# Kernel optimization log

Measured on AMD Instinct MI355X. Metric: run time of the kernel, lower is better.

The kernel has to match this reference:

```python
import jax, jax.numpy as jnp
import numpy as np

N = 50000   # nodes
E = 400000  # edges
IN_DIM, H1, H2, OUT_DIM = 512, 256, 62, 128


def _param(key, shape, scale=0.05):
    return jax.random.normal(key, shape, dtype=jnp.float32) * scale


def setup_inputs() -> dict:
    key = jax.random.key(0)
    ks = jax.random.split(key, 24)
    x = jax.random.normal(ks[0], (N, IN_DIM), dtype=jnp.float32)
    edge_index_neg = jax.random.randint(ks[1], (2, E), 0, N, dtype=jnp.int64)
    d = {
        "x": x, "edge_index_neg": edge_index_neg,
        # nn.Linear params (W stored as [in, out])
        "W1": _param(ks[2], (IN_DIM, H1)), "b1": _param(ks[3], (H1,)),
        "W2": _param(ks[4], (H1, H2)),    "b2": _param(ks[5], (H2,)),
        "W3": _param(ks[6], (H2, OUT_DIM)), "b3": _param(ks[7], (OUT_DIM,)),
        # GCNConv params: lin weight (no bias) + post-aggregation bias
        "Wg1": _param(ks[8], (H1, H1)),   "bg1": _param(ks[9], (H1,)),
        "Wg2": _param(ks[10], (H2, H2)),  "bg2": _param(ks[11], (H2,)),
        "Wg3": _param(ks[12], (OUT_DIM, OUT_DIM)), "bg3": _param(ks[13], (OUT_DIM,)),
        "Wg4": _param(ks[14], (OUT_DIM, OUT_DIM)), "bg4": _param(ks[15], (OUT_DIM,)),
        "Wg5": _param(ks[16], (OUT_DIM, OUT_DIM)), "bg5": _param(ks[17], (OUT_DIM,)),
        "Wg6": _param(ks[18], (OUT_DIM, OUT_DIM)), "bg6": _param(ks[19], (OUT_DIM,)),
    }
    return d


def _build_norm(edge_index):
    # PyG GCNConv: add self-loops, symmetric normalization D^-1/2 A D^-1/2
    loop = jnp.arange(N, dtype=edge_index.dtype)
    src = jnp.concatenate([edge_index[0], loop])
    dst = jnp.concatenate([edge_index[1], loop])
    deg = jax.ops.segment_sum(jnp.ones_like(dst, dtype=jnp.float32), dst, num_segments=N)
    dinv = jnp.where(deg > 0, jax.lax.rsqrt(jnp.maximum(deg, 1.0)), 0.0)
    norm = dinv[src] * dinv[dst]  # [E+N]
    return src, dst, norm


def _gcn(x, W, b, src, dst, norm):
    h = x @ W                                   # [N, F]
    msg = h[src] * norm[:, None]                # gather + edge scale
    out = jax.ops.segment_sum(msg, dst, num_segments=N)  # scatter-add
    return out + b


def reference(x, edge_index_neg, W1, b1, W2, b2, W3, b3,
              Wg1, bg1, Wg2, bg2, Wg3, bg3, Wg4, bg4, Wg5, bg5, Wg6, bg6):
    src, dst, norm = _build_norm(edge_index_neg)
    relu = jax.nn.relu
    x1l = x @ W1 + b1
    x1 = x1l + relu(_gcn(x1l, Wg1, bg1, src, dst, norm))
    x2l = x1 @ W2 + b2
    x2 = x2l + relu(_gcn(x2l, Wg2, bg2, src, dst, norm))
    x3l = x2 @ W3 + b3
    x3 = x3l + 0.5 * relu(_gcn(x3l, Wg3, bg3, src, dst, norm))
    x4 = x3 + 0.5 * relu(_gcn(x4_in := x3, Wg4, bg4, src, dst, norm))
    x5 = x4 + 0.25 * relu(_gcn(x4, Wg5, bg5, src, dst, norm))
    x6 = x5 + 0.25 * _gcn(x5, Wg6, bg6, src, dst, norm)
    return x6
```

## Files before the change

### kernel.cpp

```cpp
#include <hip/hip_runtime.h>

#define NN 50000
#define NE 400000
#define NBLK 196

using short8 = __attribute__((ext_vector_type(8))) short;
using f32x4  = __attribute__((ext_vector_type(4))) float;
using f32x2  = __attribute__((ext_vector_type(2))) float;
using u16x2  = __attribute__((ext_vector_type(2))) unsigned short;
using u16x4  = __attribute__((ext_vector_type(4))) unsigned short;

__device__ __forceinline__ unsigned short f2b(float f) {
    union { float f; unsigned int u; } x; x.f = f;
    unsigned int u = x.u;
    u += 0x7fffu + ((u >> 16) & 1u);
    return (unsigned short)(u >> 16);
}
__device__ __forceinline__ float b2f(unsigned short u) {
    union { unsigned int u; float f; } x; x.u = ((unsigned int)u) << 16;
    return x.f;
}

#define SWZ(b, row) ((b) ^ (((row) & 7) << 4))

__device__ __forceinline__ void gload16(const void* g, void* l) {
    __builtin_amdgcn_global_load_lds(
        (const __attribute__((address_space(1))) void*)g,
        (__attribute__((address_space(3))) void*)l, 16, 0, 0);
}

__global__ __launch_bounds__(256) void zero2_k(int* a, int* b) {
    int i = blockIdx.x * 256 + threadIdx.x;
    if (i < NN) { a[i] = 0; b[i] = 0; }
}
__global__ __launch_bounds__(256) void count_k(const int* __restrict__ dst, int* __restrict__ indeg) {
    int e = blockIdx.x * 256 + threadIdx.x;
    if (e < NE) atomicAdd(&indeg[dst[e]], 1);
}
__global__ __launch_bounds__(256) void scan1_k(const int* __restrict__ indeg, int* __restrict__ tmp,
                                               int* __restrict__ bsum) {
    __shared__ int s[256];
    int t = threadIdx.x, i = blockIdx.x * 256 + t;
    int v = (i < NN) ? indeg[i] : 0;
    s[t] = v; __syncthreads();
    for (int off = 1; off < 256; off <<= 1) {
        int x = (t >= off) ? s[t - off] : 0;
        __syncthreads();
        s[t] += x;
        __syncthreads();
    }
    if (i < NN) tmp[i] = s[t];
    if (t == 255) bsum[blockIdx.x] = s[255];
}
__global__ __launch_bounds__(256) void scan2_k(const int* __restrict__ bsum, int* __restrict__ boff) {
    __shared__ int s[256];
    int t = threadIdx.x;
    int v = (t < NBLK) ? bsum[t] : 0;
    s[t] = v; __syncthreads();
    for (int off = 1; off < 256; off <<= 1) {
        int x = (t >= off) ? s[t - off] : 0;
        __syncthreads();
        s[t] += x;
        __syncthreads();
    }
    if (t < NBLK) boff[t] = s[t] - v;
}
__global__ __launch_bounds__(256) void scan3_k(const int* __restrict__ tmp, const int* __restrict__ indeg,
                                               const int* __restrict__ boff, int* __restrict__ rowptr,
                                               float* __restrict__ dinv) {
    int i = blockIdx.x * 256 + threadIdx.x;
    if (i < NN) {
        rowptr[i] = tmp[i] - indeg[i] + boff[i >> 8];
        dinv[i] = rsqrtf((float)(1 + indeg[i]));
    }
    if (i == 0) rowptr[NN] = NE;
}
__global__ __launch_bounds__(256) void fill_k(const int* __restrict__ src, const int* __restrict__ dst,
                                              const float* __restrict__ dinv, const int* __restrict__ rowptr,
                                              int* __restrict__ cursor, int2* __restrict__ ebn) {
    int e = blockIdx.x * 256 + threadIdx.x;
    if (e >= NE) return;
    int s = src[e], d = dst[e];
    int pos = atomicAdd(&cursor[d], 1);
    ebn[rowptr[d] + pos] = make_int2(s, __float_as_int(dinv[s] * dinv[d]));
}

__global__ __launch_bounds__(256) void xcast_k(const float* __restrict__ x, unsigned short* __restrict__ xb) {
    long i = (long)blockIdx.x * 256 + threadIdx.x;
    const long total = (long)NN * 512 / 8;
    if (i >= total) return;
    float4 f0 = *(const float4*)(x + i * 8);
    float4 f1 = *(const float4*)(x + i * 8 + 4);
    short8 v;
    v[0] = (short)f2b(f0.x); v[1] = (short)f2b(f0.y);
    v[2] = (short)f2b(f0.z); v[3] = (short)f2b(f0.w);
    v[4] = (short)f2b(f1.x); v[5] = (short)f2b(f1.y);
    v[6] = (short)f2b(f1.z); v[7] = (short)f2b(f1.w);
    *(short8*)(xb + i * 8) = v;
}

struct WSegs {
    const float* W[9];
    unsigned short* Wt[9];
    int K[9], N[9], Kp[9];
    int c0[10];
};
__global__ __launch_bounds__(256) void wcast_all_k(WSegs s) {
    int blk = blockIdx.x;
    #pragma unroll
    for (int g = 0; g < 9; g++) {
        if (blk >= s.c0[g] && blk < s.c0[g + 1]) {
            int idx = (blk - s.c0[g]) * 256 + threadIdx.x;
            int Kp = s.Kp[g];
            int n = idx / Kp, k = idx % Kp;
            float v = (n < s.N[g] && k < s.K[g]) ? s.W[g][(size_t)k * s.N[g] + n] : 0.0f;
            s.Wt[g][idx] = f2b(v);
        }
    }
}

template<int BM, int BN>
__global__ __launch_bounds__(256) void gemm_mfma_k(
    const unsigned short* __restrict__ A, const unsigned short* __restrict__ Bt,
    const float* __restrict__ bias, unsigned short* __restrict__ C,
    int M, int lda, int Kp, int N, int ldc) {
    constexpr int MR = BM / 32;
    constexpr int NF = BN / 32;
    constexpr int nA = BM / 32;
    constexpr int nB = BN / 32;
    constexpr int BUFB = (BM + BN) * 128;
    __shared__ __align__(16) char lds[2 * BUFB];

    int tid = threadIdx.x;
    int lane = tid & 63, wave = tid >> 6;
    int wr = wave >> 1, wc = wave & 1;
    int lr = lane & 15, lk = lane >> 4;
    int r0 = blockIdx.x * BM, c0 = blockIdx.y * BN;

    f32x4 acc[MR][NF];
    #pragma unroll
    for (int m = 0; m < MR; m++)
        #pragma unroll
        for (int n = 0; n < NF; n++)
            acc[m][n] = (f32x4){0.f, 0.f, 0.f, 0.f};

    auto ISSUE = [&](int k0, char* buf) {
        char* AsB = buf;
        char* BsB = buf + BM * 128;
        #pragma unroll
        for (int c = 0; c < nA; c++) {
            int o = tid + c * 256;
            int row = o >> 3;
            int octg = (o & 7) ^ (row & 7);
            int gr = min(r0 + row, M - 1);
            gload16(A + (size_t)gr * lda + k0 + octg * 8, AsB + o * 16);
        }
        #pragma unroll
        for (int c = 0; c < nB; c++) {
            int o = tid + c * 256;
            int row = o >> 3;
            int octg = (o & 7) ^ (row & 7);
            gload16(Bt + (size_t)(c0 + row) * Kp + k0 + octg * 8, BsB + o * 16);
        }
    };

    int nt = Kp >> 6;
    ISSUE(0, lds);
    __syncthreads();
    for (int t = 0; t < nt; t++) {
        char* cur = lds + (t & 1) * BUFB;
        if (t + 1 < nt) ISSUE((t + 1) << 6, lds + ((t + 1) & 1) * BUFB);
        char* AsB = cur;
        char* BsB = cur + BM * 128;
        #pragma unroll
        for (int kk = 0; kk < 2; kk++) {
            int kb = kk * 64 + lk * 16;
            short8 a[MR], b[NF];
            #pragma unroll
            for (int m = 0; m < MR; m++) {
                int row = wr * (BM / 2) + m * 16 + lr;
                a[m] = *(short8*)(AsB + SWZ(row * 128 + kb, row));
            }
            #pragma unroll
            for (int n = 0; n < NF; n++) {
                int row = wc * (BN / 2) + n * 16 + lr;
                b[n] = *(short8*)(BsB + SWZ(row * 128 + kb, row));
            }
            #pragma unroll
            for (int m = 0; m < MR; m++)
                #pragma unroll
                for (int n = 0; n < NF; n++)
                    acc[m][n] = __builtin_amdgcn_mfma_f32_16x16x32_bf16(a[m], b[n], acc[m][n], 0, 0, 0);
        }
        __syncthreads();
    }

    constexpr int LDC = BN + 8;
    unsigned short* ldsC = (unsigned short*)lds;
    #pragma unroll
    for (int n = 0; n < NF; n++) {
        int cc = wc * (BN / 2) + n * 16 + lr;
        int gc = c0 + cc;
        float bv = (bias != nullptr && gc < N) ? bias[gc] : 0.0f;
        bool ok = gc < N;
        #pragma unroll
        for (int m = 0; m < MR; m++)
            #pragma unroll
            for (int j = 0; j < 4; j++) {
                int row = wr * (BM / 2) + m * 16 + lk * 4 + j;
                float v = ok ? acc[m][n][j] + bv : 0.0f;
                ldsC[row * LDC + cc] = f2b(v);
            }
    }
    __syncthreads();
    constexpr int CH = (BM * BN) / 2048;
    #pragma unroll
    for (int c = 0; c < CH; c++) {
        int o = tid + c * 256;
        int row = o / (BN / 8), col = (o % (BN / 8)) * 8;
        int gr = r0 + row;
        if (gr < M)
            *(short8*)(C + (size_t)gr * ldc + c0 + col) = *(short8*)(ldsC + row * LDC + col);
    }
}

template<int VEC> struct BV;
template<> struct BV<1> { using T = unsigned short; };
template<> struct BV<2> { using T = u16x2; };
template<> struct BV<4> { using T = u16x4; };
template<int VEC> struct FV;
template<> struct FV<1> { using T = float; };
template<> struct FV<2> { using T = f32x2; };
template<> struct FV<4> { using T = f32x4; };

template<int VEC, int SPLIT, bool OUTF32>
__global__ __launch_bounds__(256) void gather_k(
    const unsigned short* __restrict__ h, const unsigned short* __restrict__ base,
    const float* __restrict__ dinv, const float* __restrict__ bias,
    const int2* __restrict__ ebn, const int* __restrict__ rowptr,
    void* __restrict__ outraw, float alpha, int dorelu, int F) {
    constexpr int ld = 64 * VEC * SPLIT;
    int gw = (blockIdx.x * 256 + threadIdx.x) >> 6;
    int lane = threadIdx.x & 63;
    int w = gw / SPLIT;
    int colbase = (gw % SPLIT) * 64 * VEC;
    if (w >= NN) return;
    using LT = typename BV<VEC>::T;
    const int col = colbase + lane * VEC;

    float acc[VEC];
    float dn = dinv[w];
    {
        LT t = *(const LT*)(h + (size_t)w * ld + col);
        const unsigned short* tu = (const unsigned short*)&t;
        #pragma unroll
        for (int v = 0; v < VEC; v++) acc[v] = b2f(tu[v]) * dn * dn;
    }
    int e = rowptr[w], end = rowptr[w + 1];
    for (; e + 8 <= end; e += 8) {
        long long q[8];
        #pragma unroll
        for (int i = 0; i < 8; i++)
            q[i] = __builtin_nontemporal_load((const long long*)(ebn + e + i));
        LT t[8];
        #pragma unroll
        for (int i = 0; i < 8; i++)
            t[i] = *(const LT*)(h + (size_t)(int)q[i] * ld + col);
        #pragma unroll
        for (int i = 0; i < 8; i++) {
            float nr = __int_as_float((int)(q[i] >> 32));
            const unsigned short* u = (const unsigned short*)&t[i];
            #pragma unroll
            for (int v = 0; v < VEC; v++) acc[v] += b2f(u[v]) * nr;
        }
    }
    for (; e + 2 <= end; e += 2) {
        long long q0 = __builtin_nontemporal_load((const long long*)(ebn + e));
        long long q1 = __builtin_nontemporal_load((const long long*)(ebn + e + 1));
        LT t0 = *(const LT*)(h + (size_t)(int)q0 * ld + col);
        LT t1 = *(const LT*)(h + (size_t)(int)q1 * ld + col);
        float n0 = __int_as_float((int)(q0 >> 32)), n1 = __int_as_float((int)(q1 >> 32));
        const unsigned short* u0 = (const unsigned short*)&t0;
        const unsigned short* u1 = (const unsigned short*)&t1;
        #pragma unroll
        for (int v = 0; v < VEC; v++) acc[v] += b2f(u0[v]) * n0 + b2f(u1[v]) * n1;
    }
    if (e < end) {
        long long q0 = __builtin_nontemporal_load((const long long*)(ebn + e));
        LT t0 = *(const LT*)(h + (size_t)(int)q0 * ld + col);
        float n0 = __int_as_float((int)(q0 >> 32));
        const unsigned short* u0 = (const unsigned short*)&t0;
        #pragma unroll
        for (int v = 0; v < VEC; v++) acc[v] += b2f(u0[v]) * n0;
    }
    LT bt = __builtin_nontemporal_load((const LT*)(base + (size_t)w * ld + col));
    const unsigned short* bu = (const unsigned short*)&bt;
    if (OUTF32) {
        typename FV<VEC>::T ot;
        float* of = (float*)&ot;
        #pragma unroll
        for (int v = 0; v < VEC; v++) {
            int f = col + v;
            float a = acc[v] + ((f < F) ? bias[f] : 0.0f);
            if (dorelu) a = fmaxf(a, 0.0f);
            of[v] = (f < F) ? b2f(bu[v]) + alpha * a : 0.0f;
        }
        __builtin_nontemporal_store(ot, (typename FV<VEC>::T*)((float*)outraw + (size_t)w * ld + col));
    } else {
        LT ot;
        unsigned short* ou = (unsigned short*)&ot;
        #pragma unroll
        for (int v = 0; v < VEC; v++) {
            int f = col + v;
            float a = acc[v] + ((f < F) ? bias[f] : 0.0f);
            if (dorelu) a = fmaxf(a, 0.0f);
            float res = (f < F) ? b2f(bu[v]) + alpha * a : 0.0f;
            ou[v] = f2b(res);
        }
        __builtin_nontemporal_store(ot, (LT*)((unsigned short*)outraw + (size_t)w * ld + col));
    }
}

extern "C" void kernel_launch(void* const* d_in, const int* in_sizes, int n_in,
                              void* d_out, int out_size, void* d_ws, size_t ws_size,
                              hipStream_t stream) {
    const float* x   = (const float*)d_in[0];
    const int*   ei  = (const int*)d_in[1];
    const float* W1  = (const float*)d_in[2];  const float* b1  = (const float*)d_in[3];
    const float* W2  = (const float*)d_in[4];  const float* b2  = (const float*)d_in[5];
    const float* W3  = (const float*)d_in[6];  const float* b3  = (const float*)d_in[7];
    const float* Wg1 = (const float*)d_in[8];  const float* bg1 = (const float*)d_in[9];
    const float* Wg2 = (const float*)d_in[10]; const float* bg2 = (const float*)d_in[11];
    const float* Wg3 = (const float*)d_in[12]; const float* bg3 = (const float*)d_in[13];
    const float* Wg4 = (const float*)d_in[14]; const float* bg4 = (const float*)d_in[15];
    const float* Wg5 = (const float*)d_in[16]; const float* bg5 = (const float*)d_in[17];
    const float* Wg6 = (const float*)d_in[18]; const float* bg6 = (const float*)d_in[19];
    const int* srcv = ei;
    const int* dstv = ei + NE;

    float* dinv = (float*)d_ws;
    unsigned short* xb = (unsigned short*)(dinv + 51200);
    unsigned short* hA = xb + (size_t)NN * 512;
    unsigned short* hB = hA + (size_t)NN * 256;
    unsigned short* hC = hB + (size_t)NN * 256;
    unsigned short* W1t  = hC + (size_t)NN * 256;
    unsigned short* Wg1t = W1t  + 256 * 512;
    unsigned short* W2t  = Wg1t + 256 * 256;
    unsigned short* Wg2t = W2t  + 64 * 256;
    unsigned short* W3t  = Wg2t + 64 * 64;
    unsigned short* Wg3t = W3t  + 128 * 64;
    unsigned short* Wg4t = Wg3t + 128 * 128;
    unsigned short* Wg5t = Wg4t + 128 * 128;
    unsigned short* Wg6t = Wg5t + 128 * 128;
    int* indeg  = (int*)(Wg6t + 128 * 128);
    int* cursor = indeg + 51200;
    int* tmp    = cursor + 51200;
    int* rowptr = tmp + 51200;
    int* bsum   = rowptr + 51264;
    int* boff   = bsum + 256;
    int2* ebn   = (int2*)(boff + 256);

    zero2_k<<<NBLK, 256, 0, stream>>>(indeg, cursor);
    count_k<<<(NE + 255) / 256, 256, 0, stream>>>(dstv, indeg);
    scan1_k<<<NBLK, 256, 0, stream>>>(indeg, tmp, bsum);
    scan2_k<<<1, 256, 0, stream>>>(bsum, boff);
    scan3_k<<<NBLK, 256, 0, stream>>>(tmp, indeg, boff, rowptr, dinv);
    fill_k<<<(NE + 255) / 256, 256, 0, stream>>>(srcv, dstv, dinv, rowptr, cursor, ebn);

    xcast_k<<<(int)(((long)NN * 512 / 8 + 255) / 256), 256, 0, stream>>>(x, xb);

    {
        WSegs s;
        const float* Ws[9] = {W1, Wg1, W2, Wg2, W3, Wg3, Wg4, Wg5, Wg6};
        unsigned short* Wts[9] = {W1t, Wg1t, W2t, Wg2t, W3t, Wg3t, Wg4t, Wg5t, Wg6t};
        int Ks[9]  = {512, 256, 256, 62, 62, 128, 128, 128, 128};
        int Ns[9]  = {256, 256, 62, 62, 128, 128, 128, 128, 128};
        int Kps[9] = {512, 256, 256, 64, 64, 128, 128, 128, 128};
        int Nps[9] = {256, 256, 64, 64, 128, 128, 128, 128, 128};
        int c = 0;
        for (int g = 0; g < 9; g++) {
            s.W[g] = Ws[g]; s.Wt[g] = Wts[g];
            s.K[g] = Ks[g]; s.N[g] = Ns[g]; s.Kp[g] = Kps[g];
            s.c0[g] = c;
            c += (Kps[g] * Nps[g]) / 256;
        }
        s.c0[9] = c;
        wcast_all_k<<<c, 256, 0, stream>>>(s);
    }

    const int GX = (NN + 63) / 64;
    const int GG1 = (NN * 64 + 255) / 256;
    const int GG2 = (NN * 2 * 64 + 255) / 256;

    gemm_mfma_k<64, 128><<<dim3(GX, 2), 256, 0, stream>>>(xb, W1t, b1, hA, NN, 512, 512, 256, 256);
    gemm_mfma_k<64, 128><<<dim3(GX, 2), 256, 0, stream>>>(hA, Wg1t, nullptr, hB, NN, 256, 256, 256, 256);
    gather_k<2, 2, false><<<GG2, 256, 0, stream>>>(hB, hA, dinv, bg1, ebn, rowptr, hC, 1.0f, 1, 256);
    gemm_mfma_k<64, 64><<<dim3(GX, 1), 256, 0, stream>>>(hC, W2t, b2, hA, NN, 256, 256, 62, 64);
    gemm_mfma_k<64, 64><<<dim3(GX, 1), 256, 0, stream>>>(hA, Wg2t, nullptr, hB, NN, 64, 64, 62, 64);
    gather_k<1, 1, false><<<GG1, 256, 0, stream>>>(hB, hA, dinv, bg2, ebn, rowptr, hC, 1.0f, 1, 62);
    gemm_mfma_k<64, 64><<<dim3(GX, 2), 256, 0, stream>>>(hC, W3t, b3, hA, NN, 64, 64, 128, 128);
    gemm_mfma_k<64, 64><<<dim3(GX, 2), 256, 0, stream>>>(hA, Wg3t, nullptr, hB, NN, 128, 128, 128, 128);
    gather_k<2, 1, false><<<GG1, 256, 0, stream>>>(hB, hA, dinv, bg3, ebn, rowptr, hC, 0.5f, 1, 128);
    gemm_mfma_k<64, 64><<<dim3(GX, 2), 256, 0, stream>>>(hC, Wg4t, nullptr, hA, NN, 128, 128, 128, 128);
    gather_k<2, 1, false><<<GG1, 256, 0, stream>>>(hA, hC, dinv, bg4, ebn, rowptr, hB, 0.5f, 1, 128);
    gemm_mfma_k<64, 64><<<dim3(GX, 2), 256, 0, stream>>>(hB, Wg5t, nullptr, hA, NN, 128, 128, 128, 128);
    gather_k<2, 1, false><<<GG1, 256, 0, stream>>>(hA, hB, dinv, bg5, ebn, rowptr, hC, 0.25f, 1, 128);
    gemm_mfma_k<64, 64><<<dim3(GX, 2), 256, 0, stream>>>(hC, Wg6t, nullptr, hA, NN, 128, 128, 128, 128);
    gather_k<2, 1, true><<<GG1, 256, 0, stream>>>(hA, hC, dinv, bg6, ebn, rowptr, d_out, 0.25f, 0, 128);
}
```

Measured before the change: 407.6 us.

## Fuse fp32-to-bf16 input cast into first GEMM and widen N tiles

Drops the separate x cast kernel. The first GEMM now loads fp32 rows of x into registers, converts them to bf16 and writes them into swizzled LDS, which removes a full bf16 write and re-read of the 50000x512 input. The 128-wide GEMMs switch to 64x128 tiles, so each block covers all output columns and the A tile is read once. Gather kernels replace nontemporal loads and stores with plain ones. The register-staged fp32 path loses the async direct-to-LDS loads and adds register pressure.

```diff
diff --git a/kernel.cpp b/kernel.cpp
--- a/kernel.cpp
+++ b/kernel.cpp
@@ -83,20 +83,6 @@
     int s = src[e], d = dst[e];
     int pos = atomicAdd(&cursor[d], 1);
     ebn[rowptr[d] + pos] = make_int2(s, __float_as_int(dinv[s] * dinv[d]));
-}
-
-__global__ __launch_bounds__(256) void xcast_k(const float* __restrict__ x, unsigned short* __restrict__ xb) {
-    long i = (long)blockIdx.x * 256 + threadIdx.x;
-    const long total = (long)NN * 512 / 8;
-    if (i >= total) return;
-    float4 f0 = *(const float4*)(x + i * 8);
-    float4 f1 = *(const float4*)(x + i * 8 + 4);
-    short8 v;
-    v[0] = (short)f2b(f0.x); v[1] = (short)f2b(f0.y);
-    v[2] = (short)f2b(f0.z); v[3] = (short)f2b(f0.w);
-    v[4] = (short)f2b(f1.x); v[5] = (short)f2b(f1.y);
-    v[6] = (short)f2b(f1.z); v[7] = (short)f2b(f1.w);
-    *(short8*)(xb + i * 8) = v;
 }
 
 struct WSegs {
@@ -119,9 +105,9 @@
     }
 }
 
-template<int BM, int BN>
+template<bool AF32, int BM, int BN>
 __global__ __launch_bounds__(256) void gemm_mfma_k(
-    const unsigned short* __restrict__ A, const unsigned short* __restrict__ Bt,
+    const void* __restrict__ Araw, const unsigned short* __restrict__ Bt,
     const float* __restrict__ bias, unsigned short* __restrict__ C,
     int M, int lda, int Kp, int N, int ldc) {
     constexpr int MR = BM / 32;
@@ -144,6 +130,43 @@
         for (int n = 0; n < NF; n++)
             acc[m][n] = (f32x4){0.f, 0.f, 0.f, 0.f};
 
+    float4 fa0[nA], fa1[nA];
+    short8 rb_[nB];
+
+    auto LOADF = [&](int k0) {
+        #pragma unroll
+        for (int c = 0; c < nA; c++) {
+            int o = tid + c * 256, row = o >> 3, oct = o & 7;
+            int gr = min(r0 + row, M - 1);
+            const float* p = (const float*)Araw + (size_t)gr * lda + k0 + oct * 8;
+            fa0[c] = *(const float4*)p;
+            fa1[c] = *(const float4*)(p + 4);
+        }
+        #pragma unroll
+        for (int c = 0; c < nB; c++) {
+            int o = tid + c * 256, row = o >> 3, oct = o & 7;
+            rb_[c] = *(const short8*)(Bt + (size_t)(c0 + row) * Kp + k0 + oct * 8);
+        }
+    };
+    auto STOREF = [&](char* buf) {
+        char* AsB = buf;
+        char* BsB = buf + BM * 128;
+        #pragma unroll
+        for (int c = 0; c < nA; c++) {
+            int o = tid + c * 256, row = o >> 3, oct = o & 7;
+            short8 v;
+            v[0] = (short)f2b(fa0[c].x); v[1] = (short)f2b(fa0[c].y);
+            v[2] = (short)f2b(fa0[c].z); v[3] = (short)f2b(fa0[c].w);
+            v[4] = (short)f2b(fa1[c].x); v[5] = (short)f2b(fa1[c].y);
+            v[6] = (short)f2b(fa1[c].z); v[7] = (short)f2b(fa1[c].w);
+            *(short8*)(AsB + SWZ(row * 128 + oct * 16, row)) = v;
+        }
+        #pragma unroll
+        for (int c = 0; c < nB; c++) {
+            int o = tid + c * 256, row = o >> 3, oct = o & 7;
+            *(short8*)(BsB + SWZ(row * 128 + oct * 16, row)) = rb_[c];
+        }
+    };
     auto ISSUE = [&](int k0, char* buf) {
         char* AsB = buf;
         char* BsB = buf + BM * 128;
@@ -153,7 +176,7 @@
             int row = o >> 3;
             int octg = (o & 7) ^ (row & 7);
             int gr = min(r0 + row, M - 1);
-            gload16(A + (size_t)gr * lda + k0 + octg * 8, AsB + o * 16);
+            gload16((const unsigned short*)Araw + (size_t)gr * lda + k0 + octg * 8, AsB + o * 16);
         }
         #pragma unroll
         for (int c = 0; c < nB; c++) {
@@ -165,11 +188,20 @@
     };
 
     int nt = Kp >> 6;
-    ISSUE(0, lds);
+    if constexpr (AF32) {
+        LOADF(0);
+        STOREF(lds);
+    } else {
+        ISSUE(0, lds);
+    }
     __syncthreads();
     for (int t = 0; t < nt; t++) {
         char* cur = lds + (t & 1) * BUFB;
-        if (t + 1 < nt) ISSUE((t + 1) << 6, lds + ((t + 1) & 1) * BUFB);
+        char* alt = lds + ((t + 1) & 1) * BUFB;
+        if (t + 1 < nt) {
+            if constexpr (AF32) LOADF((t + 1) << 6);
+            else ISSUE((t + 1) << 6, alt);
+        }
         char* AsB = cur;
         char* BsB = cur + BM * 128;
         #pragma unroll
@@ -192,6 +224,7 @@
                 for (int n = 0; n < NF; n++)
                     acc[m][n] = __builtin_amdgcn_mfma_f32_16x16x32_bf16(a[m], b[n], acc[m][n], 0, 0, 0);
         }
+        if constexpr (AF32) { if (t + 1 < nt) STOREF(alt); }
         __syncthreads();
     }
 
@@ -293,7 +326,7 @@
         #pragma unroll
         for (int v = 0; v < VEC; v++) acc[v] += b2f(u0[v]) * n0;
     }
-    LT bt = __builtin_nontemporal_load((const LT*)(base + (size_t)w * ld + col));
+    LT bt = *(const LT*)(base + (size_t)w * ld + col);
     const unsigned short* bu = (const unsigned short*)&bt;
     if (OUTF32) {
         typename FV<VEC>::T ot;
@@ -305,7 +338,7 @@
             if (dorelu) a = fmaxf(a, 0.0f);
             of[v] = (f < F) ? b2f(bu[v]) + alpha * a : 0.0f;
         }
-        __builtin_nontemporal_store(ot, (typename FV<VEC>::T*)((float*)outraw + (size_t)w * ld + col));
+        *(typename FV<VEC>::T*)((float*)outraw + (size_t)w * ld + col) = ot;
     } else {
         LT ot;
         unsigned short* ou = (unsigned short*)&ot;
@@ -317,7 +350,7 @@
             float res = (f < F) ? b2f(bu[v]) + alpha * a : 0.0f;
             ou[v] = f2b(res);
         }
-        __builtin_nontemporal_store(ot, (LT*)((unsigned short*)outraw + (size_t)w * ld + col));
+        *(LT*)((unsigned short*)outraw + (size_t)w * ld + col) = ot;
     }
 }
 
@@ -339,8 +372,7 @@
     const int* dstv = ei + NE;
 
     float* dinv = (float*)d_ws;
-    unsigned short* xb = (unsigned short*)(dinv + 51200);
-    unsigned short* hA = xb + (size_t)NN * 512;
+    unsigned short* hA = (unsigned short*)(dinv + 51200);
     unsigned short* hB = hA + (size_t)NN * 256;
     unsigned short* hC = hB + (size_t)NN * 256;
     unsigned short* W1t  = hC + (size_t)NN * 256;
@@ -367,8 +399,6 @@
     scan3_k<<<NBLK, 256, 0, stream>>>(tmp, indeg, boff, rowptr, dinv);
     fill_k<<<(NE + 255) / 256, 256, 0, stream>>>(srcv, dstv, dinv, rowptr, cursor, ebn);
 
-    xcast_k<<<(int)(((long)NN * 512 / 8 + 255) / 256), 256, 0, stream>>>(x, xb);
-
     {
         WSegs s;
         const float* Ws[9] = {W1, Wg1, W2, Wg2, W3, Wg3, Wg4, Wg5, Wg6};
@@ -392,19 +422,19 @@
     const int GG1 = (NN * 64 + 255) / 256;
     const int GG2 = (NN * 2 * 64 + 255) / 256;
 
-    gemm_mfma_k<64, 128><<<dim3(GX, 2), 256, 0, stream>>>(xb, W1t, b1, hA, NN, 512, 512, 256, 256);
-    gemm_mfma_k<64, 128><<<dim3(GX, 2), 256, 0, stream>>>(hA, Wg1t, nullptr, hB, NN, 256, 256, 256, 256);
+    gemm_mfma_k<true, 64, 128><<<dim3(GX, 2), 256, 0, stream>>>(x, W1t, b1, hA, NN, 512, 512, 256, 256);
+    gemm_mfma_k<false, 64, 128><<<dim3(GX, 2), 256, 0, stream>>>(hA, Wg1t, nullptr, hB, NN, 256, 256, 256, 256);
     gather_k<2, 2, false><<<GG2, 256, 0, stream>>>(hB, hA, dinv, bg1, ebn, rowptr, hC, 1.0f, 1, 256);
-    gemm_mfma_k<64, 64><<<dim3(GX, 1), 256, 0, stream>>>(hC, W2t, b2, hA, NN, 256, 256, 62, 64);
-    gemm_mfma_k<64, 64><<<dim3(GX, 1), 256, 0, stream>>>(hA, Wg2t, nullptr, hB, NN, 64, 64, 62, 64);
+    gemm_mfma_k<false, 64, 64><<<dim3(GX, 1), 256, 0, stream>>>(hC, W2t, b2, hA, NN, 256, 256, 62, 64);
+    gemm_mfma_k<false, 64, 64><<<dim3(GX, 1), 256, 0, stream>>>(hA, Wg2t, nullptr, hB, NN, 64, 64, 62, 64);
     gather_k<1, 1, false><<<GG1, 256, 0, stream>>>(hB, hA, dinv, bg2, ebn, rowptr, hC, 1.0f, 1, 62);
-    gemm_mfma_k<64, 64><<<dim3(GX, 2), 256, 0, stream>>>(hC, W3t, b3, hA, NN, 64, 64, 128, 128);
-    gemm_mfma_k<64, 64><<<dim3(GX, 2), 256, 0, stream>>>(hA, Wg3t, nullptr, hB, NN, 128, 128, 128, 128);
+    gemm_mfma_k<false, 64, 128><<<dim3(GX, 1), 256, 0, stream>>>(hC, W3t, b3, hA, NN, 64, 64, 128, 128);
+    gemm_mfma_k<false, 64, 128><<<dim3(GX, 1), 256, 0, stream>>>(hA, Wg3t, nullptr, hB, NN, 128, 128, 128, 128);
     gather_k<2, 1, false><<<GG1, 256, 0, stream>>>(hB, hA, dinv, bg3, ebn, rowptr, hC, 0.5f, 1, 128);
-    gemm_mfma_k<64, 64><<<dim3(GX, 2), 256, 0, stream>>>(hC, Wg4t, nullptr, hA, NN, 128, 128, 128, 128);
+    gemm_mfma_k<false, 64, 128><<<dim3(GX, 1), 256, 0, stream>>>(hC, Wg4t, nullptr, hA, NN, 128, 128, 128, 128);
     gather_k<2, 1, false><<<GG1, 256, 0, stream>>>(hA, hC, dinv, bg4, ebn, rowptr, hB, 0.5f, 1, 128);
-    gemm_mfma_k<64, 64><<<dim3(GX, 2), 256, 0, stream>>>(hB, Wg5t, nullptr, hA, NN, 128, 128, 128, 128);
+    gemm_mfma_k<false, 64, 128><<<dim3(GX, 1), 256, 0, stream>>>(hB, Wg5t, nullptr, hA, NN, 128, 128, 128, 128);
     gather_k<2, 1, false><<<GG1, 256, 0, stream>>>(hA, hB, dinv, bg5, ebn, rowptr, hC, 0.25f, 1, 128);
-    gemm_mfma_k<64, 64><<<dim3(GX, 2), 256, 0, stream>>>(hC, Wg6t, nullptr, hA, NN, 128, 128, 128, 128);
+    gemm_mfma_k<false, 64, 128><<<dim3(GX, 1), 256, 0, stream>>>(hC, Wg6t, nullptr, hA, NN, 128, 128, 128, 128);
     gather_k<2, 1, true><<<GG1, 256, 0, stream>>>(hA, hC, dinv, bg6, ebn, rowptr, d_out, 0.25f, 0, 128);
 }
```

Measured after the change: 402.0 us. About the same (-1.4%).
